# Performance work log

Measured on AMD Instinct MI355X. Metric: run time of the kernel, lower is better.

The kernel has to match this reference:

```python
import jax, jax.numpy as jnp
import numpy as np

N = 100000          # total nodes
E = 1600000         # edges
C = 128             # in_channels
H = 256             # hidden_size
ACT_DIM = 20        # nodes per graph -> batch = N // ACT_DIM


def setup_inputs() -> dict:
    key = jax.random.key(0)
    ks = jax.random.split(key, 10)
    x = jax.random.normal(ks[0], (N, C), dtype=jnp.float32)
    edge_index = jax.random.randint(ks[1], (2, E), 0, N, dtype=jnp.int64)
    s = 0.05
    conv_w = jax.random.normal(ks[2], (C, C), dtype=jnp.float32) * s   # [in, out]
    conv_b = jnp.zeros((C,), dtype=jnp.float32)
    lin1_w = jax.random.normal(ks[3], (H, C), dtype=jnp.float32) * s   # torch [out, in]
    lin1_b = jnp.zeros((H,), dtype=jnp.float32)
    lin2_w = jax.random.normal(ks[4], (H, H), dtype=jnp.float32) * s
    lin2_b = jnp.zeros((H,), dtype=jnp.float32)
    lin3_w = jax.random.normal(ks[5], (1, H), dtype=jnp.float32) * s
    lin3_b = jnp.zeros((1,), dtype=jnp.float32)
    return {"x": x, "edge_index": edge_index,
            "conv_w": conv_w, "conv_b": conv_b,
            "lin1_w": lin1_w, "lin1_b": lin1_b,
            "lin2_w": lin2_w, "lin2_b": lin2_b,
            "lin3_w": lin3_w, "lin3_b": lin3_b}


def gcn_conv(x, edge_index, w, b):
    """PyG GCNConv: x' = D^{-1/2} (A + I) D^{-1/2} (x W) + b."""
    n = x.shape[0]
    loops = jnp.arange(n, dtype=edge_index.dtype)
    src = jnp.concatenate([edge_index[0], loops])  # [E + N]
    dst = jnp.concatenate([edge_index[1], loops])
    deg = jax.ops.segment_sum(jnp.ones_like(dst, dtype=x.dtype), dst, num_segments=n)
    dinv = jnp.where(deg > 0, jax.lax.rsqrt(deg), 0.0)
    norm = dinv[src] * dinv[dst]                   # [E + N]
    xw = x @ w                                     # [N, out]
    msg = xw[src] * norm[:, None]                  # gather + scale, [E+N, out]
    out = jax.ops.segment_sum(msg, dst, num_segments=n)  # scatter-add
    return out + b


def reference(x, edge_index, conv_w, conv_b, lin1_w, lin1_b, lin2_w, lin2_b, lin3_w, lin3_b):
    out = jax.nn.relu(gcn_conv(x, edge_index, conv_w, conv_b))
    h = out + x                                    # residual, [N, C]
    h = h.reshape(-1, ACT_DIM, C)                  # [B, act_dim, C]
    h = jax.nn.relu(h @ lin1_w.T + lin1_b)         # [B, act_dim, H]
    h = jax.nn.relu(h @ lin2_w.T + lin2_b)
    h = jnp.sum(h, axis=1)                         # [B, H]
    h = h @ lin3_w.T + lin3_b                      # [B, 1]
    if h.shape[0] == 1:                            # torch .squeeze(0) semantics
        h = h[0]
    return h
```

## Files before the change

### kernel.cpp

```cpp
#include <hip/hip_runtime.h>
#include <hip/hip_bf16.h>
#include <cstddef>

#define NNODES 100000
#define NEDGES 1600000
#define CIN 128
#define HID 256
#define ACT 20
#define NGRAPH (NNODES / ACT)
#define BSHIFT 8
#define NB ((NNODES + 255) >> 8)
#define BIN_WGS 512
#define CAP 8192

typedef __attribute__((ext_vector_type(8))) short short8;
typedef __attribute__((ext_vector_type(4))) float f32x4;

__device__ __forceinline__ unsigned short f2b(float f) {
    unsigned u = __float_as_uint(f);
    u += 0x7FFF + ((u >> 16) & 1);
    return (unsigned short)(u >> 16);
}
__device__ __forceinline__ float b2f(unsigned short h) {
    return __uint_as_float(((unsigned)h) << 16);
}


__global__ __launch_bounds__(256) void bin_k(const int* __restrict__ ei,
                                             int* __restrict__ bfill,
                                             unsigned* __restrict__ entries) {
    __shared__ int cnt[NB], base[NB], cur[NB];
    for (int i = threadIdx.x; i < NB; i += 256) { cnt[i] = 0; cur[i] = 0; }
    __syncthreads();
    const int per = NEDGES / BIN_WGS;
    const int s = blockIdx.x * per;
    const int e = s + per;
    for (int i = s + threadIdx.x; i < e; i += 256)
        atomicAdd(&cnt[ei[NEDGES + i] >> BSHIFT], 1);
    __syncthreads();
    for (int i = threadIdx.x; i < NB; i += 256)
        base[i] = cnt[i] ? atomicAdd(&bfill[i], cnt[i]) : 0;
    __syncthreads();
    for (int i = s + threadIdx.x; i < e; i += 256) {
        int src = ei[i], dst = ei[NEDGES + i];
        int b = dst >> BSHIFT;
        int r = base[b] + atomicAdd(&cur[b], 1);
        if (r < CAP)
            entries[(size_t)b * CAP + r] = ((unsigned)src << 8) | (unsigned)(dst & 255);
    }
}

__global__ __launch_bounds__(256) void bucket_build_k(
    const unsigned* __restrict__ entries, const int* __restrict__ bfill,
    int2* __restrict__ rowptr2, int* __restrict__ csr, float* __restrict__ dinv) {
    const int b = blockIdx.x;
    const int count = min(bfill[b], CAP);
    const int node0 = b << BSHIFT;
    const int nn = min(256, NNODES - node0);
    const size_t gbase = (size_t)b * CAP;
    __shared__ int cnt[256], off[256], cur[256];
    const int t = threadIdx.x;
    cnt[t] = 0; cur[t] = 0;
    __syncthreads();
    for (int i = t; i < count; i += 256)
        atomicAdd(&cnt[entries[gbase + i] & 255], 1);
    __syncthreads();
    int lane = t & 63, wid = t >> 6;
    int v = cnt[t];
    int inc = v;
#pragma unroll
    for (int o = 1; o < 64; o <<= 1) {
        int tv = __shfl_up(inc, o, 64);
        if (lane >= o) inc += tv;
    }
    __shared__ int wsum[4];
    if (lane == 63) wsum[wid] = inc;
    __syncthreads();
    int woff = 0;
#pragma unroll
    for (int w = 0; w < 4; ++w) woff += (w < wid) ? wsum[w] : 0;
    int excl = inc + woff - v;
    off[t] = excl;
    if (t < nn) {
        rowptr2[node0 + t] = make_int2((int)gbase + excl, (int)gbase + excl + v);
        dinv[node0 + t] = rsqrtf(1.0f + (float)v);
    }
    __syncthreads();
    for (int i = t; i < count; i += 256) {
        unsigned en = entries[gbase + i];
        int loc = (int)(en & 255);
        int r = atomicAdd(&cur[loc], 1);
        csr[gbase + off[loc] + r] = (int)(en >> 8);
    }
}


__global__ void cvt_w_k(const float* __restrict__ conv_w,
                        const float* __restrict__ lin1_w,
                        const float* __restrict__ lin2_w,
                        unsigned short* __restrict__ wt0,
                        unsigned short* __restrict__ wt1,
                        unsigned short* __restrict__ wt2) {
    int id = blockIdx.x * 256 + threadIdx.x;
    if (id < 16384) {
        int k = id >> 7, n = id & 127;
        wt0[n * 128 + k] = f2b(conv_w[k * 128 + n]);
    } else if (id < 16384 + 32768) {
        int i = id - 16384;
        wt1[i] = f2b(lin1_w[i]);
    } else if (id < 16384 + 32768 + 65536) {
        int i = id - 49152;
        wt2[i] = f2b(lin2_w[i]);
    }
}


__global__ __launch_bounds__(256) void mgemm0_k(
    const float* __restrict__ Af, const unsigned short* __restrict__ B,
    const float* __restrict__ dinv, unsigned short* __restrict__ Cout, int M)
{
    const int tid = threadIdx.x;
    const int wid = tid >> 6;
    const int lane = tid & 63;
    const int quad = lane >> 4;
    const int l16 = lane & 15;
    const int bm = blockIdx.x * 128 + (wid >> 1) * 64;
    const int bn = (wid & 1) * 64;

    const float* pa[4];
    const unsigned short* pb[4];
#pragma unroll
    for (int t = 0; t < 4; ++t) {
        int m = bm + t * 16 + l16; if (m >= M) m = M - 1;
        pa[t] = Af + (size_t)m * 128 + quad * 8;
        int n = bn + t * 16 + l16;
        pb[t] = B + (size_t)n * 128 + quad * 8;
    }

    f32x4 acc[4][4];
#pragma unroll
    for (int i = 0; i < 4; ++i)
#pragma unroll
        for (int j = 0; j < 4; ++j) {
            f32x4 z = {0.f, 0.f, 0.f, 0.f};
            acc[i][j] = z;
        }

    float4 afl[2][4][2];
    short8 bf[2][4];
#pragma unroll
    for (int t = 0; t < 4; ++t) {
        afl[0][t][0] = *reinterpret_cast<const float4*>(pa[t]);
        afl[0][t][1] = *reinterpret_cast<const float4*>(pa[t] + 4);
        bf[0][t] = *reinterpret_cast<const short8*>(pb[t]);
    }

#pragma unroll
    for (int kt = 0; kt < 4; ++kt) {
        const int cur = kt & 1, nxt = cur ^ 1;
        if (kt < 3) {
#pragma unroll
            for (int t = 0; t < 4; ++t) {
                afl[nxt][t][0] = *reinterpret_cast<const float4*>(pa[t] + (kt + 1) * 32);
                afl[nxt][t][1] = *reinterpret_cast<const float4*>(pa[t] + (kt + 1) * 32 + 4);
                bf[nxt][t] = *reinterpret_cast<const short8*>(pb[t] + (kt + 1) * 32);
            }
        }
        short8 a[4];
#pragma unroll
        for (int t = 0; t < 4; ++t) {
            float4 f0 = afl[cur][t][0], f1 = afl[cur][t][1];
            short8 av;
            av[0] = (short)f2b(f0.x); av[1] = (short)f2b(f0.y);
            av[2] = (short)f2b(f0.z); av[3] = (short)f2b(f0.w);
            av[4] = (short)f2b(f1.x); av[5] = (short)f2b(f1.y);
            av[6] = (short)f2b(f1.z); av[7] = (short)f2b(f1.w);
            a[t] = av;
        }
#pragma unroll
        for (int i = 0; i < 4; ++i)
#pragma unroll
            for (int j = 0; j < 4; ++j)
                acc[i][j] = __builtin_amdgcn_mfma_f32_16x16x32_bf16(a[i], bf[cur][j], acc[i][j], 0, 0, 0);
    }

#pragma unroll
    for (int i = 0; i < 4; ++i)
#pragma unroll
        for (int r = 0; r < 4; ++r) {
            int row = bm + i * 16 + quad * 4 + r;
            if (row >= M) continue;
            float dv = dinv[row];
#pragma unroll
            for (int j = 0; j < 4; ++j) {
                int col = bn + j * 16 + l16;
                Cout[(size_t)row * 128 + col] = f2b(acc[i][j][r] * dv);
            }
        }
}


__global__ __launch_bounds__(256) void gather_k(
    const int2* __restrict__ rowptr2, const int* __restrict__ csr,
    const unsigned short* __restrict__ xws, const float* __restrict__ dinv,
    const float* __restrict__ x, const float* __restrict__ conv_b,
    unsigned short* __restrict__ h0)
{
    const int node = blockIdx.x * 4 + (threadIdx.x >> 6);
    if (node >= NNODES) return;
    const int lane = threadIdx.x & 63;
    const int sub = lane >> 4;
    const int c16 = lane & 15;

    const int2 se = rowptr2[node];
    const int start = se.x, end = se.y;

    float2 s2[4];
    if (sub == 0) {
        uint4 v = *reinterpret_cast<const uint4*>(xws + (size_t)node * CIN + c16 * 8);
        unsigned d[4] = {v.x, v.y, v.z, v.w};
#pragma unroll
        for (int k = 0; k < 4; ++k) {
            s2[k].x = __uint_as_float(d[k] << 16);
            s2[k].y = __uint_as_float(d[k] & 0xffff0000u);
        }
    } else {
#pragma unroll
        for (int k = 0; k < 4; ++k) s2[k] = make_float2(0.f, 0.f);
    }

    for (int p = start; p < end; p += 32) {
        uint4 r[8];
        int valid[8];
#pragma unroll
        for (int j = 0; j < 8; ++j) {
            int e = p + j * 4 + sub;
            bool a = e < end;
            int idx = a ? csr[e] : node;
            r[j] = *reinterpret_cast<const uint4*>(xws + (size_t)idx * CIN + c16 * 8);
            valid[j] = a;
        }
#pragma unroll
        for (int j = 0; j < 8; ++j)
            if (valid[j]) {
                unsigned d[4] = {r[j].x, r[j].y, r[j].z, r[j].w};
#pragma unroll
                for (int k = 0; k < 4; ++k) {
                    s2[k].x += __uint_as_float(d[k] << 16);
                    s2[k].y += __uint_as_float(d[k] & 0xffff0000u);
                }
            }
    }

#pragma unroll
    for (int k = 0; k < 4; ++k) {
        s2[k].x += __shfl_xor(s2[k].x, 16, 64);
        s2[k].y += __shfl_xor(s2[k].y, 16, 64);
        s2[k].x += __shfl_xor(s2[k].x, 32, 64);
        s2[k].y += __shfl_xor(s2[k].y, 32, 64);
    }

    if (sub == 0) {
        float dvv = dinv[node];
        float4 b0 = *reinterpret_cast<const float4*>(conv_b + c16 * 8);
        float4 b1 = *reinterpret_cast<const float4*>(conv_b + c16 * 8 + 4);
        float4 x0 = *reinterpret_cast<const float4*>(x + (size_t)node * CIN + c16 * 8);
        float4 x1 = *reinterpret_cast<const float4*>(x + (size_t)node * CIN + c16 * 8 + 4);
        float o[8];
        o[0] = fmaxf(s2[0].x * dvv + b0.x, 0.f) + x0.x;
        o[1] = fmaxf(s2[0].y * dvv + b0.y, 0.f) + x0.y;
        o[2] = fmaxf(s2[1].x * dvv + b0.z, 0.f) + x0.z;
        o[3] = fmaxf(s2[1].y * dvv + b0.w, 0.f) + x0.w;
        o[4] = fmaxf(s2[2].x * dvv + b1.x, 0.f) + x1.x;
        o[5] = fmaxf(s2[2].y * dvv + b1.y, 0.f) + x1.y;
        o[6] = fmaxf(s2[3].x * dvv + b1.z, 0.f) + x1.z;
        o[7] = fmaxf(s2[3].y * dvv + b1.w, 0.f) + x1.w;
        short8 pk;
#pragma unroll
        for (int q = 0; q < 8; ++q) pk[q] = (short)f2b(o[q]);
        *reinterpret_cast<short8*>(h0 + (size_t)node * CIN + c16 * 8) = pk;
    }
}


__global__ __launch_bounds__(256) void fmlp_k(
    const unsigned short* __restrict__ h0, const unsigned short* __restrict__ w1,
    const float* __restrict__ b1, const unsigned short* __restrict__ w2,
    const float* __restrict__ b2, const float* __restrict__ w3,
    float* __restrict__ rowsum, int M)
{
    __shared__ unsigned short h1s[64 * 256];
    const int tid = threadIdx.x;
    const int wave = tid >> 6;
    const int lane = tid & 63;
    const int quad = lane >> 4;
    const int l16 = lane & 15;
    const int bm = blockIdx.x * 64;
    const int nc0 = wave * 64;

    f32x4 acc[4][4];
#pragma unroll
    for (int i = 0; i < 4; ++i)
#pragma unroll
        for (int j = 0; j < 4; ++j) {
            f32x4 z = {0.f, 0.f, 0.f, 0.f};
            acc[i][j] = z;
        }

    {
        const unsigned short* pa[4];
        const unsigned short* pb[4];
#pragma unroll
        for (int t = 0; t < 4; ++t) {
            int m = bm + t * 16 + l16; if (m >= M) m = M - 1;
            pa[t] = h0 + (size_t)m * 128 + quad * 8;
            int n = nc0 + t * 16 + l16;
            pb[t] = w1 + (size_t)n * 128 + quad * 8;
        }
        short8 af[2][4], bf[2][4];
#pragma unroll
        for (int t = 0; t < 4; ++t) {
            af[0][t] = *reinterpret_cast<const short8*>(pa[t]);
            bf[0][t] = *reinterpret_cast<const short8*>(pb[t]);
        }
#pragma unroll
        for (int kt = 0; kt < 4; ++kt) {
            const int cur = kt & 1, nxt = cur ^ 1;
            if (kt < 3) {
#pragma unroll
                for (int t = 0; t < 4; ++t) {
                    af[nxt][t] = *reinterpret_cast<const short8*>(pa[t] + (kt + 1) * 32);
                    bf[nxt][t] = *reinterpret_cast<const short8*>(pb[t] + (kt + 1) * 32);
                }
            }
#pragma unroll
            for (int i = 0; i < 4; ++i)
#pragma unroll
                for (int j = 0; j < 4; ++j)
                    acc[i][j] = __builtin_amdgcn_mfma_f32_16x16x32_bf16(af[cur][i], bf[cur][j], acc[i][j], 0, 0, 0);
        }
#pragma unroll
        for (int nt = 0; nt < 4; ++nt) {
            int col = nc0 + nt * 16 + l16;
            float bv = b1[col];
            int chunk = col >> 3, rem = col & 7;
#pragma unroll
            for (int mt = 0; mt < 4; ++mt)
#pragma unroll
                for (int r = 0; r < 4; ++r) {
                    int row = mt * 16 + quad * 4 + r;
                    h1s[row * 256 + (((chunk ^ (row & 7)) << 3) | rem)] =
                        f2b(fmaxf(acc[mt][nt][r] + bv, 0.f));
                }
        }
    }
    __syncthreads();

#pragma unroll
    for (int i = 0; i < 4; ++i)
#pragma unroll
        for (int j = 0; j < 4; ++j) {
            f32x4 z = {0.f, 0.f, 0.f, 0.f};
            acc[i][j] = z;
        }
    {
        const unsigned short* pb[4];
#pragma unroll
        for (int t = 0; t < 4; ++t) {
            int n = nc0 + t * 16 + l16;
            pb[t] = w2 + (size_t)n * 256 + quad * 8;
        }
        short8 af[2][4], bf[2][4];
#pragma unroll
        for (int t = 0; t < 4; ++t) {
            int row = t * 16 + l16;
            af[0][t] = *reinterpret_cast<const short8*>(
                &h1s[row * 256 + (((quad ^ (row & 7)) << 3))]);
            bf[0][t] = *reinterpret_cast<const short8*>(pb[t]);
        }
#pragma unroll
        for (int kt = 0; kt < 8; ++kt) {
            const int cur = kt & 1, nxt = cur ^ 1;
            if (kt < 7) {
                const int c1 = (kt + 1) * 4 + quad;
#pragma unroll
                for (int t = 0; t < 4; ++t) {
                    int row = t * 16 + l16;
                    af[nxt][t] = *reinterpret_cast<const short8*>(
                        &h1s[row * 256 + ((c1 ^ (row & 7)) << 3)]);
                    bf[nxt][t] = *reinterpret_cast<const short8*>(pb[t] + (kt + 1) * 32);
                }
            }
#pragma unroll
            for (int i = 0; i < 4; ++i)
#pragma unroll
                for (int j = 0; j < 4; ++j)
                    acc[i][j] = __builtin_amdgcn_mfma_f32_16x16x32_bf16(af[cur][i], bf[cur][j], acc[i][j], 0, 0, 0);
        }
    }

    float part[4][4];
#pragma unroll
    for (int mt = 0; mt < 4; ++mt)
#pragma unroll
        for (int r = 0; r < 4; ++r) part[mt][r] = 0.f;
#pragma unroll
    for (int nt = 0; nt < 4; ++nt) {
        int col = nc0 + nt * 16 + l16;
        float bs = b2[col];
        float wv3 = w3[col];
#pragma unroll
        for (int mt = 0; mt < 4; ++mt)
#pragma unroll
            for (int r = 0; r < 4; ++r)
                part[mt][r] += fmaxf(acc[mt][nt][r] + bs, 0.f) * wv3;
    }
#pragma unroll
    for (int mt = 0; mt < 4; ++mt)
#pragma unroll
        for (int r = 0; r < 4; ++r) {
            float v = part[mt][r];
            v += __shfl_xor(v, 1, 64);
            v += __shfl_xor(v, 2, 64);
            v += __shfl_xor(v, 4, 64);
            v += __shfl_xor(v, 8, 64);
            part[mt][r] = v;
        }
    if (l16 == 0) {
#pragma unroll
        for (int mt = 0; mt < 4; ++mt)
#pragma unroll
            for (int r = 0; r < 4; ++r) {
                int row = bm + mt * 16 + quad * 4 + r;
                if (row < M) rowsum[(size_t)row * 4 + wave] = part[mt][r];
            }
    }
}


__global__ __launch_bounds__(256) void final_k(
    const float* __restrict__ rowsum, const float* __restrict__ b3,
    float* __restrict__ out)
{
    int g = blockIdx.x * 256 + threadIdx.x;
    if (g >= NGRAPH) return;
    const float4* p = reinterpret_cast<const float4*>(rowsum + (size_t)g * 80);
    float s = 0.f;
#pragma unroll
    for (int i = 0; i < 20; ++i) {
        float4 v = p[i];
        s += (v.x + v.y) + (v.z + v.w);
    }
    out[g] = s + b3[0];
}


extern "C" void kernel_launch(void* const* d_in, const int* in_sizes, int n_in,
                              void* d_out, int out_size, void* d_ws, size_t ws_size,
                              hipStream_t stream)
{
    const float* x      = (const float*)d_in[0];
    const int*   ei     = (const int*)  d_in[1];
    const float* conv_w = (const float*)d_in[2];
    const float* conv_b = (const float*)d_in[3];
    const float* lin1_w = (const float*)d_in[4];
    const float* lin1_b = (const float*)d_in[5];
    const float* lin2_w = (const float*)d_in[6];
    const float* lin2_b = (const float*)d_in[7];
    const float* lin3_w = (const float*)d_in[8];
    const float* lin3_b = (const float*)d_in[9];
    float* out = (float*)d_out;

    unsigned short* xws     = (unsigned short*)d_ws;
    unsigned short* h0      = xws + (size_t)12800000;
    unsigned*       entries = (unsigned*)(h0 + (size_t)12800000);
    int*            csr     = (int*)(entries + (size_t)NB * CAP);
    int2*           rowptr2 = (int2*)(csr + (size_t)NB * CAP);
    float*          dinv    = (float*)(rowptr2 + NNODES);
    int*            bfill   = (int*)(dinv + NNODES);
    unsigned short* wt0     = (unsigned short*)(bfill + NB + 8);
    unsigned short* wt1     = wt0 + 16384;
    unsigned short* wt2     = wt1 + 32768;
    float*          rowsum  = (float*)(wt2 + 65536);

    hipMemsetAsync(bfill, 0, NB * sizeof(int), stream);
    bin_k<<<BIN_WGS, 256, 0, stream>>>(ei, bfill, entries);
    bucket_build_k<<<NB, 256, 0, stream>>>(entries, bfill, rowptr2, csr, dinv);

    cvt_w_k<<<(114688 + 255) / 256, 256, 0, stream>>>(conv_w, lin1_w, lin2_w, wt0, wt1, wt2);

    mgemm0_k<<<(NNODES + 127) / 128, 256, 0, stream>>>(x, wt0, dinv, xws, NNODES);

    gather_k<<<(NNODES + 3) / 4, 256, 0, stream>>>(rowptr2, csr, xws, dinv, x, conv_b, h0);

    fmlp_k<<<(NNODES + 63) / 64, 256, 0, stream>>>(h0, wt1, lin1_b, wt2, lin2_b, lin3_w,
                                                   rowsum, NNODES);

    final_k<<<(NGRAPH + 255) / 256, 256, 0, stream>>>(rowsum, lin3_b, out);
}
```

Before: 310.7 us.

## Stage binned edges in LDS for coalesced writes; triple-buffer lin2 MFMA operands

The binning kernel now computes per-workgroup bucket offsets with a wave-level prefix scan. It stages the packed edge entries and their global destinations in shared memory, then writes them out in a linear pass. This replaces scattered per-edge global writes with writes grouped by bucket, at the cost of extra LDS (two PER_WG arrays) and an extra barrier. The lin2 MFMA loop also moves from double to triple buffering, prefetching two k-steps ahead, which raises register pressure.

After: 308.3 us. About the same (-0.8%).

```diff
diff --git a/kernel.cpp b/kernel.cpp
--- a/kernel.cpp
+++ b/kernel.cpp
@@ -11,6 +11,7 @@
 #define BSHIFT 8
 #define NB ((NNODES + 255) >> 8)
 #define BIN_WGS 512
+#define PER_WG (NEDGES / BIN_WGS)
 #define CAP 8192
 
 typedef __attribute__((ext_vector_type(8))) short short8;
@@ -29,24 +30,53 @@
 __global__ __launch_bounds__(256) void bin_k(const int* __restrict__ ei,
                                              int* __restrict__ bfill,
                                              unsigned* __restrict__ entries) {
-    __shared__ int cnt[NB], base[NB], cur[NB];
-    for (int i = threadIdx.x; i < NB; i += 256) { cnt[i] = 0; cur[i] = 0; }
-    __syncthreads();
-    const int per = NEDGES / BIN_WGS;
-    const int s = blockIdx.x * per;
-    const int e = s + per;
-    for (int i = s + threadIdx.x; i < e; i += 256)
+    __shared__ int cnt[NB], lofs[NB], base[NB], cur[NB];
+    __shared__ unsigned lbuf[PER_WG];
+    __shared__ int gdst[PER_WG];
+    __shared__ int wsum[4];
+    const int t = threadIdx.x;
+    for (int i = t; i < NB; i += 256) { cnt[i] = 0; cur[i] = 0; }
+    __syncthreads();
+    const int s = blockIdx.x * PER_WG;
+    const int e = s + PER_WG;
+    for (int i = s + t; i < e; i += 256)
         atomicAdd(&cnt[ei[NEDGES + i] >> BSHIFT], 1);
     __syncthreads();
-    for (int i = threadIdx.x; i < NB; i += 256)
-        base[i] = cnt[i] ? atomicAdd(&bfill[i], cnt[i]) : 0;
-    __syncthreads();
-    for (int i = s + threadIdx.x; i < e; i += 256) {
+    int c0 = (2 * t < NB) ? cnt[2 * t] : 0;
+    int c1 = (2 * t + 1 < NB) ? cnt[2 * t + 1] : 0;
+    int v = c0 + c1;
+    int lane = t & 63, wid = t >> 6;
+    int inc = v;
+#pragma unroll
+    for (int o = 1; o < 64; o <<= 1) {
+        int tv = __shfl_up(inc, o, 64);
+        if (lane >= o) inc += tv;
+    }
+    if (lane == 63) wsum[wid] = inc;
+    __syncthreads();
+    int woff = 0;
+#pragma unroll
+    for (int w = 0; w < 4; ++w) woff += (w < wid) ? wsum[w] : 0;
+    int excl = inc + woff - v;
+    if (2 * t < NB) lofs[2 * t] = excl;
+    if (2 * t + 1 < NB) lofs[2 * t + 1] = excl + c0;
+    __syncthreads();
+    for (int b = t; b < NB; b += 256)
+        base[b] = cnt[b] ? atomicAdd(&bfill[b], cnt[b]) : 0;
+    __syncthreads();
+    for (int i = s + t; i < e; i += 256) {
         int src = ei[i], dst = ei[NEDGES + i];
         int b = dst >> BSHIFT;
-        int r = base[b] + atomicAdd(&cur[b], 1);
-        if (r < CAP)
-            entries[(size_t)b * CAP + r] = ((unsigned)src << 8) | (unsigned)(dst & 255);
+        int r = atomicAdd(&cur[b], 1);
+        int slot = lofs[b] + r;
+        lbuf[slot] = ((unsigned)src << 8) | (unsigned)(dst & 255);
+        int g = base[b] + r;
+        gdst[slot] = (g < CAP) ? (int)((size_t)b * CAP + g) : -1;
+    }
+    __syncthreads();
+    for (int i = t; i < PER_WG; i += 256) {
+        int g = gdst[i];
+        if (g >= 0) entries[g] = lbuf[i];
     }
 }
 
@@ -370,32 +400,35 @@
             int n = nc0 + t * 16 + l16;
             pb[t] = w2 + (size_t)n * 256 + quad * 8;
         }
-        short8 af[2][4], bf[2][4];
+        short8 af[3][4], bf[3][4];
 #pragma unroll
         for (int t = 0; t < 4; ++t) {
             int row = t * 16 + l16;
             af[0][t] = *reinterpret_cast<const short8*>(
-                &h1s[row * 256 + (((quad ^ (row & 7)) << 3))]);
+                &h1s[row * 256 + ((quad ^ (row & 7)) << 3)]);
+            af[1][t] = *reinterpret_cast<const short8*>(
+                &h1s[row * 256 + (((4 + quad) ^ (row & 7)) << 3)]);
             bf[0][t] = *reinterpret_cast<const short8*>(pb[t]);
+            bf[1][t] = *reinterpret_cast<const short8*>(pb[t] + 32);
         }
 #pragma unroll
         for (int kt = 0; kt < 8; ++kt) {
-            const int cur = kt & 1, nxt = cur ^ 1;
-            if (kt < 7) {
-                const int c1 = (kt + 1) * 4 + quad;
+            const int cu = kt % 3, nx = (kt + 2) % 3;
+            if (kt + 2 < 8) {
+                const int c2 = (kt + 2) * 4 + quad;
 #pragma unroll
                 for (int t = 0; t < 4; ++t) {
                     int row = t * 16 + l16;
-                    af[nxt][t] = *reinterpret_cast<const short8*>(
-                        &h1s[row * 256 + ((c1 ^ (row & 7)) << 3)]);
-                    bf[nxt][t] = *reinterpret_cast<const short8*>(pb[t] + (kt + 1) * 32);
+                    af[nx][t] = *reinterpret_cast<const short8*>(
+                        &h1s[row * 256 + ((c2 ^ (row & 7)) << 3)]);
+                    bf[nx][t] = *reinterpret_cast<const short8*>(pb[t] + (kt + 2) * 32);
                 }
             }
 #pragma unroll
             for (int i = 0; i < 4; ++i)
 #pragma unroll
                 for (int j = 0; j < 4; ++j)
-                    acc[i][j] = __builtin_amdgcn_mfma_f32_16x16x32_bf16(af[cur][i], bf[cur][j], acc[i][j], 0, 0, 0);
+                    acc[i][j] = __builtin_amdgcn_mfma_f32_16x16x32_bf16(af[cu][i], bf[cu][j], acc[i][j], 0, 0, 0);
         }
     }
 
```
